# Kernel tuning notes

Hardware: AMD Instinct MI355X
Metric: run time of the kernel (lower is better)

## Reference

```python
import jax, jax.numpy as jnp
import numpy as np

B, C, H, W, MODES = 16, 64, 256, 256, 12
BN_EPS = 1e-5


def setup_inputs() -> dict:
    key = jax.random.key(0)
    ks = jax.random.split(key, 5)
    scale = 1.0 / (C * C)
    return {
        "x": jax.random.normal(ks[0], (B, C, H, W), jnp.float32),
        "w1": scale * jax.random.normal(ks[1], (C, C, MODES, MODES, 2), jnp.float32),
        "w2": scale * jax.random.normal(ks[2], (C, C, MODES, MODES, 2), jnp.float32),
        "wc": jax.random.normal(ks[3], (C, C), jnp.float32) / np.sqrt(C),
        "bc": jax.random.normal(ks[4], (C,), jnp.float32) * 0.01,
        "gamma": jnp.ones((C,), jnp.float32),
        "beta": jnp.zeros((C,), jnp.float32),
    }


def _spectral_conv2d(x, w1, w2):
    # x: [B, C, H, W] -> rfft2 -> truncated complex mode multiply -> irfft2
    b, c, h, w = x.shape
    m = w1.shape[2]
    xf = jnp.fft.rfft2(x)  # [B, C, H, W//2+1] complex64
    cw1 = w1[..., 0] + 1j * w1[..., 1]  # [Cin, Cout, m, m]
    cw2 = w2[..., 0] + 1j * w2[..., 1]
    top = jnp.einsum("bixy,ioxy->boxy", xf[:, :, :m, :m], cw1)
    bot = jnp.einsum("bixy,ioxy->boxy", xf[:, :, -m:, :m], cw2)
    out_ft = (
        jnp.zeros((b, c, h, w // 2 + 1), jnp.complex64)
        .at[:, :, :m, :m].set(top)
        .at[:, :, -m:, :m].set(bot)
    )
    return jnp.fft.irfft2(out_ft, s=(h, w))


def reference(x, w1, w2, wc, bc, gamma, beta):
    # fftconv(x) + 1x1 conv(x)
    y = _spectral_conv2d(x, w1, w2)
    y = y + jnp.einsum("bihw,oi->bohw", x, wc) + bc[None, :, None, None]
    # BatchNorm2d (training mode: batch statistics, biased variance)
    mean = y.mean(axis=(0, 2, 3), keepdims=True)
    var = y.var(axis=(0, 2, 3), keepdims=True)
    y = (y - mean) * jax.lax.rsqrt(var + BN_EPS)
    y = y * gamma[None, :, None, None] + beta[None, :, None, None]
    # exact GELU (torch nn.GELU default uses erf)
    return jax.nn.gelu(y, approximate=False)
```

## Files before the change

### kernel.cpp

```cpp
#include <hip/hip_runtime.h>
#include <math.h>

#define NB 16
#define NC 64
#define NH 256
#define NW 256
#define NM 12
#define NJ 24
#define NMODE 288
#define TPI256 0.024543692606170254f

#define WS_STATS   0
#define WS_STATS2  128
#define WS_EW      256
#define WS_EH      (WS_EW + 6144)
#define WS_XW      (WS_EH + 12288)
#define WS_XF      (WS_XW + 6291456)
#define WS_F       (WS_XF + 589824)
#define WS_Y1      (WS_F  + 589824)
#define WS_TOTAL   (WS_Y1 + 6291456)

__global__ __launch_bounds__(256) void k0_init(float* __restrict__ ws) {
    int t = blockIdx.x * 256 + threadIdx.x;
    if (t < 128) ws[WS_STATS + t] = 0.f;
    if (t < 12 * 256) {
        int kx = t >> 8, w = t & 255;
        float ang = (float)((kx * w) & 255) * TPI256;
        float s, c; sincosf(ang, &s, &c);
        ws[WS_EW + t * 2] = c; ws[WS_EW + t * 2 + 1] = s;
    }
    if (t < 24 * 256) {
        int j = t >> 8, h = t & 255;
        int ky = (j < 12) ? j : (232 + j);
        float ang = (float)((ky * h) & 255) * TPI256;
        float s, c; sincosf(ang, &s, &c);
        ws[WS_EH + t * 2] = c; ws[WS_EH + t * 2 + 1] = s;
    }
}

__global__ __launch_bounds__(256) void k1_dftw(const float* __restrict__ x,
                                               float* __restrict__ ws) {
    __shared__ float xs[32 * 260];
    const float* ew = ws + WS_EW;
    float* xw = ws + WS_XW;
    int t = threadIdx.x;
    int rowbase = blockIdx.x * 32;
    const float4* src = (const float4*)(x + (size_t)rowbase * 256);
#pragma unroll
    for (int k = 0; k < 8; k++) {
        int g = t + 256 * k;
        int r = g >> 6, q = g & 63;
        ((float4*)(xs + r * 260))[q] = src[g];
    }
    __syncthreads();
    for (int item = t; item < 384; item += 256) {
        int r = item / 12, kx = item - r * 12;
        const float4* xr = (const float4*)(xs + r * 260);
        const float4* ewr = (const float4*)(ew + kx * 512);
        float are = 0.f, aim = 0.f;
#pragma unroll 4
        for (int q = 0; q < 64; q++) {
            float4 xv = xr[q];
            float4 e0 = ewr[2 * q];
            float4 e1 = ewr[2 * q + 1];
            are += xv.x * e0.x + xv.y * e0.z + xv.z * e1.x + xv.w * e1.z;
            aim -= xv.x * e0.y + xv.y * e0.w + xv.z * e1.y + xv.w * e1.w;
        }
        int R = rowbase + r;
        ((float2*)xw)[R * 12 + kx] = make_float2(are, aim);
    }
}

__global__ __launch_bounds__(256) void k2_dfth(float* __restrict__ ws) {
    __shared__ float sxw[256 * 24];
    int t = threadIdx.x;
    int bc = blockIdx.x;
    const float* eh = ws + WS_EH;
    const float4* src = (const float4*)(ws + WS_XW + (size_t)bc * 6144);
#pragma unroll
    for (int k = 0; k < 6; k++) ((float4*)sxw)[t + 256 * k] = src[t + 256 * k];
    __syncthreads();
    float2* xf = (float2*)(ws + WS_XF) + (size_t)bc * 288;
    for (int m = t; m < 288; m += 256) {
        int j = m / 12, kx = m - j * 12;
        const float2* ej = (const float2*)(eh + j * 512);
        float re = 0.f, im = 0.f;
#pragma unroll 4
        for (int h = 0; h < 256; h++) {
            float2 e = ej[h];
            float2 xv = ((const float2*)sxw)[h * 12 + kx];
            re += xv.x * e.x + xv.y * e.y;
            im += xv.y * e.x - xv.x * e.y;
        }
        xf[m] = make_float2(re, im);
    }
}

__global__ __launch_bounds__(256) void k3_mix(const float* __restrict__ w1,
                                              const float* __restrict__ w2,
                                              float* __restrict__ ws) {
    __shared__ float swg[4096 * 2];
    __shared__ float sx[1024 * 2];
    int m = blockIdx.x;
    int j = m / 12, kx = m - j * 12;
    int xm = (j < 12) ? j : (j - 12);
    const float* wsrc = (j < 12) ? w1 : w2;
    int t = threadIdx.x;
#pragma unroll
    for (int rep = 0; rep < 16; rep++) {
        int p = t + 256 * rep;
        ((float2*)swg)[p] = ((const float2*)wsrc)[p * 144 + xm * 12 + kx];
    }
    const float2* xfp = (const float2*)(ws + WS_XF);
#pragma unroll
    for (int rep = 0; rep < 4; rep++) {
        int q = t + 256 * rep;
        ((float2*)sx)[q] = xfp[q * 288 + m];
    }
    __syncthreads();
    int o = t & 63, bg = t >> 6;
    float2 acc[4];
#pragma unroll
    for (int bb = 0; bb < 4; bb++) acc[bb] = make_float2(0.f, 0.f);
    for (int i = 0; i < 64; i++) {
        float2 wv = ((const float2*)swg)[i * 64 + o];
#pragma unroll
        for (int bb = 0; bb < 4; bb++) {
            float2 xv = ((const float2*)sx)[(bb * 4 + bg) * 64 + i];
            acc[bb].x += xv.x * wv.x - xv.y * wv.y;
            acc[bb].y += xv.x * wv.y + xv.y * wv.x;
        }
    }
    float2* F = (float2*)(ws + WS_F);
#pragma unroll
    for (int bb = 0; bb < 4; bb++) {
        int b = bb * 4 + bg;
        F[(b * 288 + m) * 64 + o] = acc[bb];
    }
}

__global__ __launch_bounds__(256) void k4_idfth(float* __restrict__ ws) {
    __shared__ float2 sf[288];
    int t = threadIdx.x;
    int bo = blockIdx.x;
    int b = bo >> 6, o = bo & 63;
    const float2* F = (const float2*)(ws + WS_F);
    for (int m = t; m < 288; m += 256) sf[m] = F[(b * 288 + m) * 64 + o];
    __syncthreads();
    int h = t;
    float yr[12], yi[12];
#pragma unroll
    for (int kx = 0; kx < 12; kx++) { yr[kx] = 0.f; yi[kx] = 0.f; }
    for (int j = 0; j < 24; j++) {
        int ky = (j < 12) ? j : (232 + j);
        float ang = (float)((ky * h) & 255) * TPI256;
        float s, c; sincosf(ang, &s, &c);
#pragma unroll
        for (int kx = 0; kx < 12; kx++) {
            float2 f = sf[j * 12 + kx];
            yr[kx] += f.x * c - f.y * s;
            yi[kx] += f.x * s + f.y * c;
        }
    }
    float4* y1 = (float4*)(ws + WS_Y1 + ((size_t)bo * 256 + h) * 24);
    y1[0] = make_float4(yr[0], yi[0], yr[1], yi[1]);
    y1[1] = make_float4(yr[2], yi[2], yr[3], yi[3]);
    y1[2] = make_float4(yr[4], yi[4], yr[5], yi[5]);
    y1[3] = make_float4(yr[6], yi[6], yr[7], yi[7]);
    y1[4] = make_float4(yr[8], yi[8], yr[9], yi[9]);
    y1[5] = make_float4(yr[10], yi[10], yr[11], yi[11]);
}

__global__ __launch_bounds__(256) void k5_fuse(const float* __restrict__ x,
                                               const float* __restrict__ wc,
                                               const float* __restrict__ bcv,
                                               const float* __restrict__ ws,
                                               float* __restrict__ out) {
    __shared__ float swc[4096];
    __shared__ float sy1[64 * 24];
    __shared__ float sbc[64];
    int t = threadIdx.x;
    int bh = blockIdx.x;
    int b = bh >> 8, h = bh & 255;
#pragma unroll
    for (int k = 0; k < 16; k++) swc[t + 256 * k] = wc[t + 256 * k];
    if (t < 64) sbc[t] = bcv[t];
    const float* y1b = ws + WS_Y1 + ((size_t)b * 64 * 256 + h) * 24;
#pragma unroll
    for (int k = 0; k < 6; k++) {
        int f = t + 256 * k;
        int o = f / 24, r = f - o * 24;
        sy1[f] = y1b[(size_t)o * 6144 + r];
    }
    __syncthreads();
    int w = t;
    float xr[64];
    const float* xp = x + ((size_t)b * 64 * 256 + h) * 256 + w;
#pragma unroll
    for (int i = 0; i < 64; i++) xr[i] = xp[(size_t)i * 65536];
    float cw2[12], sw2[12];
#pragma unroll
    for (int kx = 1; kx < 12; kx++) {
        float ang = (float)((kx * w) & 255) * TPI256;
        float s, c; sincosf(ang, &s, &c);
        cw2[kx] = 2.f * c; sw2[kx] = 2.f * s;
    }
    float* outp = out + ((size_t)b * 64 * 256 + h) * 256 + w;
    const float inv = 1.f / 65536.f;
    for (int o = 0; o < 64; o++) {
        const float4* yo4 = (const float4*)(sy1 + o * 24);
        float4 a0 = yo4[0], a1 = yo4[1], a2 = yo4[2];
        float4 a3 = yo4[3], a4 = yo4[4], a5 = yo4[5];
        float spec = a0.x
            + (a0.z * cw2[1] - a0.w * sw2[1])
            + (a1.x * cw2[2] - a1.y * sw2[2])
            + (a1.z * cw2[3] - a1.w * sw2[3])
            + (a2.x * cw2[4] - a2.y * sw2[4])
            + (a2.z * cw2[5] - a2.w * sw2[5])
            + (a3.x * cw2[6] - a3.y * sw2[6])
            + (a3.z * cw2[7] - a3.w * sw2[7])
            + (a4.x * cw2[8] - a4.y * sw2[8])
            + (a4.z * cw2[9] - a4.w * sw2[9])
            + (a5.x * cw2[10] - a5.y * sw2[10])
            + (a5.z * cw2[11] - a5.w * sw2[11]);
        float acc = sbc[o] + spec * inv;
        const float4* wo = (const float4*)(swc + o * 64);
#pragma unroll
        for (int ii = 0; ii < 16; ii++) {
            float4 wv = wo[ii];
            acc += xr[4 * ii] * wv.x + xr[4 * ii + 1] * wv.y
                 + xr[4 * ii + 2] * wv.z + xr[4 * ii + 3] * wv.w;
        }
        outp[(size_t)o * 65536] = acc;
    }
}

__global__ __launch_bounds__(256) void k6_stats(const float* __restrict__ y,
                                                float* __restrict__ ws) {
    int t = threadIdx.x;
    int ob = blockIdx.x;
    const float4* p = (const float4*)(y + (size_t)ob * 65536);
    float s = 0.f, q = 0.f;
#pragma unroll 8
    for (int k = 0; k < 64; k++) {
        float4 v = p[t + 256 * k];
        s += v.x + v.y + v.z + v.w;
        q += v.x * v.x + v.y * v.y + v.z * v.z + v.w * v.w;
    }
#pragma unroll
    for (int m = 32; m; m >>= 1) { s += __shfl_xor(s, m); q += __shfl_xor(q, m); }
    __shared__ float red[8];
    int wid = t >> 6;
    if ((t & 63) == 0) { red[wid * 2] = s; red[wid * 2 + 1] = q; }
    __syncthreads();
    if (t == 0) {
        s = red[0] + red[2] + red[4] + red[6];
        q = red[1] + red[3] + red[5] + red[7];
        int o = ob & 63;
        atomicAdd(ws + WS_STATS + o, s);
        atomicAdd(ws + WS_STATS + 64 + o, q);
    }
}

__global__ void k6b_final(const float* __restrict__ gamma,
                          const float* __restrict__ beta,
                          float* __restrict__ ws) {
    int o = threadIdx.x;
    if (o < 64) {
        const float n = 1048576.f;
        float mean = ws[WS_STATS + o] / n;
        float var = ws[WS_STATS + 64 + o] / n - mean * mean;
        float a = gamma[o] * rsqrtf(var + 1e-5f);
        ws[WS_STATS2 + o] = a;
        ws[WS_STATS2 + 64 + o] = beta[o] - mean * a;
    }
}

__global__ __launch_bounds__(256) void k7_bngelu(float* __restrict__ y,
                                                 const float* __restrict__ ws) {
    const float* st = ws + WS_STATS2;
    size_t idx = (size_t)blockIdx.x * 256 + threadIdx.x;
    size_t stride = (size_t)gridDim.x * 256;
    float4* p = (float4*)y;
    for (size_t i = idx; i < 16777216u; i += stride) {
        int o = (int)((i >> 14) & 63);
        float a = st[o], bb = st[64 + o];
        float4 v = p[i];
        float z0 = a * v.x + bb, z1 = a * v.y + bb, z2 = a * v.z + bb, z3 = a * v.w + bb;
        v.x = 0.5f * z0 * (1.f + erff(z0 * 0.70710678118654752f));
        v.y = 0.5f * z1 * (1.f + erff(z1 * 0.70710678118654752f));
        v.z = 0.5f * z2 * (1.f + erff(z2 * 0.70710678118654752f));
        v.w = 0.5f * z3 * (1.f + erff(z3 * 0.70710678118654752f));
        p[i] = v;
    }
}

extern "C" void kernel_launch(void* const* d_in, const int* in_sizes, int n_in,
                              void* d_out, int out_size, void* d_ws, size_t ws_size,
                              hipStream_t stream) {
    (void)in_sizes; (void)n_in; (void)out_size;
    if (ws_size < (size_t)WS_TOTAL * sizeof(float)) return;
    const float* x     = (const float*)d_in[0];
    const float* w1    = (const float*)d_in[1];
    const float* w2    = (const float*)d_in[2];
    const float* wc    = (const float*)d_in[3];
    const float* bcv   = (const float*)d_in[4];
    const float* gamma = (const float*)d_in[5];
    const float* beta  = (const float*)d_in[6];
    float* out = (float*)d_out;
    float* ws = (float*)d_ws;

    k0_init  <<<24,   256, 0, stream>>>(ws);
    k1_dftw  <<<8192, 256, 0, stream>>>(x, ws);
    k2_dfth  <<<1024, 256, 0, stream>>>(ws);
    k3_mix   <<<288,  256, 0, stream>>>(w1, w2, ws);
    k4_idfth <<<1024, 256, 0, stream>>>(ws);
    k5_fuse  <<<4096, 256, 0, stream>>>(x, wc, bcv, ws, out);
    k6_stats <<<1024, 256, 0, stream>>>(out, ws);
    k6b_final<<<1,    64,  0, stream>>>(gamma, beta, ws);
    k7_bngelu<<<4096, 256, 0, stream>>>(out, ws);
}
```

Before: 1.602 ms.

## Register-tile width DFT, split twiddle planes, use table twiddles across kernels

The twiddle tables now store cosine and sine as separate planes. The width-DFT kernel is register-tiled: each thread accumulates 8 rows by 3 modes over staged 64-column chunks and combines partial sums with cross-lane shuffles. The height-DFT kernel now runs 288 threads so one thread owns each mode, staging twiddles through LDS. The inverse-height and fused kernels read twiddles from the tables instead of calling sincosf. The fused kernel drops its LDS staging of wc, bias and spectral rows in favour of direct global or scalar loads, which may cost bandwidth or increase register pressure.

```diff
diff --git a/kernel.cpp b/kernel.cpp
--- a/kernel.cpp
+++ b/kernel.cpp
@@ -27,73 +27,131 @@
         int kx = t >> 8, w = t & 255;
         float ang = (float)((kx * w) & 255) * TPI256;
         float s, c; sincosf(ang, &s, &c);
-        ws[WS_EW + t * 2] = c; ws[WS_EW + t * 2 + 1] = s;
+        ws[WS_EW + kx * 512 + w] = c;
+        ws[WS_EW + kx * 512 + 256 + w] = s;
     }
     if (t < 24 * 256) {
         int j = t >> 8, h = t & 255;
         int ky = (j < 12) ? j : (232 + j);
         float ang = (float)((ky * h) & 255) * TPI256;
         float s, c; sincosf(ang, &s, &c);
-        ws[WS_EH + t * 2] = c; ws[WS_EH + t * 2 + 1] = s;
+        ws[WS_EH + j * 512 + h] = c;
+        ws[WS_EH + j * 512 + 256 + h] = s;
     }
 }
 
 __global__ __launch_bounds__(256) void k1_dftw(const float* __restrict__ x,
                                                float* __restrict__ ws) {
-    __shared__ float xs[32 * 260];
-    const float* ew = ws + WS_EW;
-    float* xw = ws + WS_XW;
-    int t = threadIdx.x;
-    int rowbase = blockIdx.x * 32;
-    const float4* src = (const float4*)(x + (size_t)rowbase * 256);
-#pragma unroll
-    for (int k = 0; k < 8; k++) {
-        int g = t + 256 * k;
-        int r = g >> 6, q = g & 63;
-        ((float4*)(xs + r * 260))[q] = src[g];
-    }
-    __syncthreads();
-    for (int item = t; item < 384; item += 256) {
-        int r = item / 12, kx = item - r * 12;
-        const float4* xr = (const float4*)(xs + r * 260);
-        const float4* ewr = (const float4*)(ew + kx * 512);
-        float are = 0.f, aim = 0.f;
+    __shared__ float xs[128 * 68];
+    __shared__ float tws[12 * 136];
+    int t = threadIdx.x;
+    int wseg = t & 3, kxg = (t >> 2) & 3, r8 = t >> 4;
+    int rowbase = blockIdx.x * 128;
+    float ar[8][3], ai[8][3];
+#pragma unroll
+    for (int j = 0; j < 8; ++j)
+#pragma unroll
+        for (int i = 0; i < 3; ++i) { ar[j][i] = 0.f; ai[j][i] = 0.f; }
+
+    for (int pass = 0; pass < 4; ++pass) {
+        if (pass) __syncthreads();
+        {
+            const float* xg = x + (size_t)rowbase * 256 + pass * 64;
+            int q = t & 15, r0 = t >> 4;
+#pragma unroll
+            for (int i = 0; i < 8; ++i) {
+                int row = r0 + 16 * i;
+                *(float4*)(xs + row * 68 + q * 4) =
+                    *(const float4*)(xg + (size_t)row * 256 + q * 4);
+            }
+        }
+        for (int f = t; f < 384; f += 256) {
+            int kx = f >> 5, plane = (f >> 4) & 1, q = f & 15;
+            *(float4*)(tws + kx * 136 + plane * 68 + q * 4) =
+                *(const float4*)(ws + WS_EW + kx * 512 + plane * 256 + pass * 64 + q * 4);
+        }
+        __syncthreads();
+#pragma unroll
+        for (int wq = 0; wq < 4; ++wq) {
+            int woff = wseg * 16 + wq * 4;
+            float4 xv[8];
+#pragma unroll
+            for (int j = 0; j < 8; ++j)
+                xv[j] = *(const float4*)(xs + (r8 + 16 * j) * 68 + woff);
+#pragma unroll
+            for (int i = 0; i < 3; ++i) {
+                int kx = kxg * 3 + i;
+                float4 c4 = *(const float4*)(tws + kx * 136 + woff);
+                float4 s4 = *(const float4*)(tws + kx * 136 + 68 + woff);
+#pragma unroll
+                for (int j = 0; j < 8; ++j) {
+                    ar[j][i] += xv[j].x * c4.x + xv[j].y * c4.y + xv[j].z * c4.z + xv[j].w * c4.w;
+                    ai[j][i] -= xv[j].x * s4.x + xv[j].y * s4.y + xv[j].z * s4.z + xv[j].w * s4.w;
+                }
+            }
+        }
+    }
+#pragma unroll
+    for (int j = 0; j < 8; ++j)
+#pragma unroll
+        for (int i = 0; i < 3; ++i) {
+            ar[j][i] += __shfl_xor(ar[j][i], 1);
+            ar[j][i] += __shfl_xor(ar[j][i], 2);
+            ai[j][i] += __shfl_xor(ai[j][i], 1);
+            ai[j][i] += __shfl_xor(ai[j][i], 2);
+        }
+    if (wseg == 0) {
+        float2* xw = (float2*)(ws + WS_XW);
+#pragma unroll
+        for (int j = 0; j < 8; ++j) {
+            size_t row = rowbase + r8 + 16 * j;
+#pragma unroll
+            for (int i = 0; i < 3; ++i) {
+                int kx = kxg * 3 + i;
+                xw[row * 12 + kx] = make_float2(ar[j][i], ai[j][i]);
+            }
+        }
+    }
+}
+
+__global__ __launch_bounds__(288) void k2_dfth(float* __restrict__ ws) {
+    __shared__ float sxw[256 * 28];
+    __shared__ float ehs[24 * 136];
+    int t = threadIdx.x;
+    int bc = blockIdx.x;
+    {
+        const float4* src = (const float4*)(ws + WS_XW + (size_t)bc * 6144);
+        for (int f = t; f < 1536; f += 288) {
+            int row = f / 6, q = f - row * 6;
+            *(float4*)(sxw + row * 28 + q * 4) = src[f];
+        }
+    }
+    int j = t / 12, kx = t - j * 12;
+    float re = 0.f, im = 0.f;
+    for (int pass = 0; pass < 4; ++pass) {
+        __syncthreads();
+        for (int f = t; f < 768; f += 288) {
+            int jj = f >> 5, plane = (f >> 4) & 1, q = f & 15;
+            *(float4*)(ehs + jj * 136 + plane * 68 + q * 4) =
+                *(const float4*)(ws + WS_EH + jj * 512 + plane * 256 + pass * 64 + q * 4);
+        }
+        __syncthreads();
 #pragma unroll 4
-        for (int q = 0; q < 64; q++) {
-            float4 xv = xr[q];
-            float4 e0 = ewr[2 * q];
-            float4 e1 = ewr[2 * q + 1];
-            are += xv.x * e0.x + xv.y * e0.z + xv.z * e1.x + xv.w * e1.z;
-            aim -= xv.x * e0.y + xv.y * e0.w + xv.z * e1.y + xv.w * e1.w;
-        }
-        int R = rowbase + r;
-        ((float2*)xw)[R * 12 + kx] = make_float2(are, aim);
-    }
-}
-
-__global__ __launch_bounds__(256) void k2_dfth(float* __restrict__ ws) {
-    __shared__ float sxw[256 * 24];
-    int t = threadIdx.x;
-    int bc = blockIdx.x;
-    const float* eh = ws + WS_EH;
-    const float4* src = (const float4*)(ws + WS_XW + (size_t)bc * 6144);
-#pragma unroll
-    for (int k = 0; k < 6; k++) ((float4*)sxw)[t + 256 * k] = src[t + 256 * k];
-    __syncthreads();
-    float2* xf = (float2*)(ws + WS_XF) + (size_t)bc * 288;
-    for (int m = t; m < 288; m += 256) {
-        int j = m / 12, kx = m - j * 12;
-        const float2* ej = (const float2*)(eh + j * 512);
-        float re = 0.f, im = 0.f;
-#pragma unroll 4
-        for (int h = 0; h < 256; h++) {
-            float2 e = ej[h];
-            float2 xv = ((const float2*)sxw)[h * 12 + kx];
-            re += xv.x * e.x + xv.y * e.y;
-            im += xv.y * e.x - xv.x * e.y;
-        }
-        xf[m] = make_float2(re, im);
-    }
+        for (int hh = 0; hh < 64; hh += 4) {
+            float4 c4 = *(const float4*)(ehs + j * 136 + hh);
+            float4 s4 = *(const float4*)(ehs + j * 136 + 68 + hh);
+            int hbase = pass * 64 + hh;
+            float2 x0 = *(const float2*)(sxw + (hbase + 0) * 28 + kx * 2);
+            float2 x1 = *(const float2*)(sxw + (hbase + 1) * 28 + kx * 2);
+            float2 x2 = *(const float2*)(sxw + (hbase + 2) * 28 + kx * 2);
+            float2 x3 = *(const float2*)(sxw + (hbase + 3) * 28 + kx * 2);
+            re += x0.x * c4.x + x0.y * s4.x + x1.x * c4.y + x1.y * s4.y
+                + x2.x * c4.z + x2.y * s4.z + x3.x * c4.w + x3.y * s4.w;
+            im += x0.y * c4.x - x0.x * s4.x + x1.y * c4.y - x1.x * s4.y
+                + x2.y * c4.z - x2.x * s4.z + x3.y * c4.w - x3.x * s4.w;
+        }
+    }
+    ((float2*)(ws + WS_XF))[(size_t)bc * 288 + t] = make_float2(re, im);
 }
 
 __global__ __launch_bounds__(256) void k3_mix(const float* __restrict__ w1,
@@ -135,7 +193,7 @@
 #pragma unroll
     for (int bb = 0; bb < 4; bb++) {
         int b = bb * 4 + bg;
-        F[(b * 288 + m) * 64 + o] = acc[bb];
+        F[((size_t)b * 288 + m) * 64 + o] = acc[bb];
     }
 }
 
@@ -145,16 +203,16 @@
     int bo = blockIdx.x;
     int b = bo >> 6, o = bo & 63;
     const float2* F = (const float2*)(ws + WS_F);
-    for (int m = t; m < 288; m += 256) sf[m] = F[(b * 288 + m) * 64 + o];
+    for (int m = t; m < 288; m += 256) sf[m] = F[((size_t)b * 288 + m) * 64 + o];
     __syncthreads();
     int h = t;
     float yr[12], yi[12];
 #pragma unroll
     for (int kx = 0; kx < 12; kx++) { yr[kx] = 0.f; yi[kx] = 0.f; }
+    const float* ehp = ws + WS_EH;
     for (int j = 0; j < 24; j++) {
-        int ky = (j < 12) ? j : (232 + j);
-        float ang = (float)((ky * h) & 255) * TPI256;
-        float s, c; sincosf(ang, &s, &c);
+        float c = ehp[j * 512 + h];
+        float s = ehp[j * 512 + 256 + h];
 #pragma unroll
         for (int kx = 0; kx < 12; kx++) {
             float2 f = sf[j * 12 + kx];
@@ -176,61 +234,33 @@
                                                const float* __restrict__ bcv,
                                                const float* __restrict__ ws,
                                                float* __restrict__ out) {
-    __shared__ float swc[4096];
-    __shared__ float sy1[64 * 24];
-    __shared__ float sbc[64];
     int t = threadIdx.x;
     int bh = blockIdx.x;
     int b = bh >> 8, h = bh & 255;
-#pragma unroll
-    for (int k = 0; k < 16; k++) swc[t + 256 * k] = wc[t + 256 * k];
-    if (t < 64) sbc[t] = bcv[t];
-    const float* y1b = ws + WS_Y1 + ((size_t)b * 64 * 256 + h) * 24;
-#pragma unroll
-    for (int k = 0; k < 6; k++) {
-        int f = t + 256 * k;
-        int o = f / 24, r = f - o * 24;
-        sy1[f] = y1b[(size_t)o * 6144 + r];
-    }
-    __syncthreads();
     int w = t;
+    const float* xp = x + ((size_t)b * 64 * 256 + h) * 256 + w;
     float xr[64];
-    const float* xp = x + ((size_t)b * 64 * 256 + h) * 256 + w;
-#pragma unroll
-    for (int i = 0; i < 64; i++) xr[i] = xp[(size_t)i * 65536];
+#pragma unroll
+    for (int i = 0; i < 64; ++i) xr[i] = xp[(size_t)i * 65536];
     float cw2[12], sw2[12];
 #pragma unroll
-    for (int kx = 1; kx < 12; kx++) {
-        float ang = (float)((kx * w) & 255) * TPI256;
-        float s, c; sincosf(ang, &s, &c);
-        cw2[kx] = 2.f * c; sw2[kx] = 2.f * s;
-    }
+    for (int kx = 1; kx < 12; ++kx) {
+        cw2[kx] = 2.f * ws[WS_EW + kx * 512 + w];
+        sw2[kx] = 2.f * ws[WS_EW + kx * 512 + 256 + w];
+    }
+    const float inv = 1.f / 65536.f;
     float* outp = out + ((size_t)b * 64 * 256 + h) * 256 + w;
-    const float inv = 1.f / 65536.f;
-    for (int o = 0; o < 64; o++) {
-        const float4* yo4 = (const float4*)(sy1 + o * 24);
-        float4 a0 = yo4[0], a1 = yo4[1], a2 = yo4[2];
-        float4 a3 = yo4[3], a4 = yo4[4], a5 = yo4[5];
-        float spec = a0.x
-            + (a0.z * cw2[1] - a0.w * sw2[1])
-            + (a1.x * cw2[2] - a1.y * sw2[2])
-            + (a1.z * cw2[3] - a1.w * sw2[3])
-            + (a2.x * cw2[4] - a2.y * sw2[4])
-            + (a2.z * cw2[5] - a2.w * sw2[5])
-            + (a3.x * cw2[6] - a3.y * sw2[6])
-            + (a3.z * cw2[7] - a3.w * sw2[7])
-            + (a4.x * cw2[8] - a4.y * sw2[8])
-            + (a4.z * cw2[9] - a4.w * sw2[9])
-            + (a5.x * cw2[10] - a5.y * sw2[10])
-            + (a5.z * cw2[11] - a5.w * sw2[11]);
-        float acc = sbc[o] + spec * inv;
-        const float4* wo = (const float4*)(swc + o * 64);
-#pragma unroll
-        for (int ii = 0; ii < 16; ii++) {
-            float4 wv = wo[ii];
-            acc += xr[4 * ii] * wv.x + xr[4 * ii + 1] * wv.y
-                 + xr[4 * ii + 2] * wv.z + xr[4 * ii + 3] * wv.w;
-        }
+    const float* y1base = ws + WS_Y1 + (size_t)b * 64 * 6144 + h * 24;
+    for (int o = 0; o < 64; ++o) {
+        const float* yo = y1base + (size_t)o * 6144;
+        float spec = yo[0];
+#pragma unroll
+        for (int kx = 1; kx < 12; ++kx)
+            spec += yo[2 * kx] * cw2[kx] - yo[2 * kx + 1] * sw2[kx];
+        float acc = bcv[o] + spec * inv;
+        const float* wo = wc + o * 64;
+#pragma unroll
+        for (int ii = 0; ii < 64; ++ii) acc += xr[ii] * wo[ii];
         outp[(size_t)o * 65536] = acc;
     }
 }
@@ -311,8 +341,8 @@
     float* ws = (float*)d_ws;
 
     k0_init  <<<24,   256, 0, stream>>>(ws);
-    k1_dftw  <<<8192, 256, 0, stream>>>(x, ws);
-    k2_dfth  <<<1024, 256, 0, stream>>>(ws);
+    k1_dftw  <<<2048, 256, 0, stream>>>(x, ws);
+    k2_dfth  <<<1024, 288, 0, stream>>>(ws);
     k3_mix   <<<288,  256, 0, stream>>>(w1, w2, ws);
     k4_idfth <<<1024, 256, 0, stream>>>(ws);
     k5_fuse  <<<4096, 256, 0, stream>>>(x, wc, bcv, ws, out);
```

New measurement: 1.362 ms. 1.18x faster.
